# Kernel tuning notes

Measured on AMD Instinct MI355X. Metric: run time of the kernel, lower is better.

The kernel has to match this reference:

```python
import jax, jax.numpy as jnp
import numpy as np

B, T, H, U, F, K, M = 64, 2048, 1024, 128, 32, 31, 512
PAD = 2 * (K - 1) // 2  # dilation=2, 'same' padding = 30


def setup_inputs() -> dict:
    key = jax.random.key(0)
    ks = jax.random.split(key, 10)
    s = lambda d: 1.0 / np.sqrt(d)
    return {
        "query": jax.random.normal(ks[0], (B, 1, H), dtype=jnp.float32),
        "state": jax.random.uniform(ks[1], (B, T), dtype=jnp.float32),
        "prev_cum": jnp.zeros((B, T), dtype=jnp.float32),
        "memory": jax.random.normal(ks[2], (B, T, M), dtype=jnp.float32),
        "Wq": jax.random.normal(ks[3], (H, U), dtype=jnp.float32) * s(H),
        "bq": jnp.zeros((U,), dtype=jnp.float32),
        "Wm": jax.random.normal(ks[4], (M, U), dtype=jnp.float32) * s(M),
        "bm": jnp.zeros((U,), dtype=jnp.float32),
        "Wl": jax.random.normal(ks[5], (F, U), dtype=jnp.float32) * s(F),
        "bl": jnp.zeros((U,), dtype=jnp.float32),
        "We": jax.random.normal(ks[6], (U, U), dtype=jnp.float32) * s(U),
        "be": jnp.zeros((U,), dtype=jnp.float32),
        "va": jax.random.normal(ks[7], (U,), dtype=jnp.float32),
        "conv_w": jax.random.normal(ks[8], (F, 1, K), dtype=jnp.float32) * s(K),
        "conv_b": jnp.zeros((F,), dtype=jnp.float32),
    }


def reference(query, state, prev_cum, memory, Wq, bq, Wm, bm, Wl, bl, We, be, va, conv_w, conv_b):
    # query projection, keep first time step: [B,1,U]
    pq = (query @ Wq + bq)[:, 0:1, :]
    # processed memory (done in initialize() in torch): [B,T,U]
    pm = memory @ Wm + bm
    # location features: dilated conv over previous alignment, 'same' length
    x = state[:, None, :]  # [B,1,T]
    f = jax.lax.conv_general_dilated(
        x, conv_w, window_strides=(1,), padding=[(PAD, PAD)],
        rhs_dilation=(2,), dimension_numbers=("NCH", "OIH", "NCH"),
    ) + conv_b[None, :, None]                     # [B,F,T]
    pl = jnp.transpose(f, (0, 2, 1)) @ Wl + bl    # [B,T,U]
    # additive energy with extra linear + v_a reduction: [B,T]
    energy = jnp.sum(va * jnp.tanh((pq + pl + pm) @ We + be), axis=2)
    # smoothing (sigmoid) normalization instead of softmax
    sg = jax.nn.sigmoid(energy)
    alignment = sg / jnp.sum(sg, axis=-1, keepdims=True)  # [B,T]
    cum = prev_cum + alignment  # cumulate_weights=True
    # context over PROCESSED memory, matching self.memoery usage: [B,1,U]
    context = cum[:, None, :] @ pm
    return context
```

## Files before the change

kernel.cpp:

```cpp
#include <hip/hip_runtime.h>

#define Bv 64
#define Tv 2048
#define Hv 1024
#define Uv 128
#define Mv 512

typedef __bf16 bf16x8 __attribute__((ext_vector_type(8)));
typedef float f32x4 __attribute__((ext_vector_type(4)));

union U4BF { uint4 u; bf16x8 b; };

#define MFMA(a, b, c) __builtin_amdgcn_mfma_f32_16x16x32_bf16((a), (b), (c), 0, 0, 0)

#define GLOAD_LDS16(g, l) __builtin_amdgcn_global_load_lds( \
    (const __attribute__((address_space(1))) unsigned int*)(g), \
    (__attribute__((address_space(3))) unsigned int*)(l), 16, 0, 0)

__device__ __forceinline__ unsigned short f2bf(float f) {
  __bf16 h = (__bf16)f;
  return __builtin_bit_cast(unsigned short, h);
}
__device__ __forceinline__ unsigned int pack2(unsigned short lo, unsigned short hi) {
  return (unsigned int)lo | ((unsigned int)hi << 16);
}

__global__ __launch_bounds__(128) void k1_kernel(const float* __restrict__ query,
                                                 const float* __restrict__ Wq,
                                                 const float* __restrict__ bq,
                                                 const float* __restrict__ Wl,
                                                 const float* __restrict__ bl,
                                                 const float* __restrict__ conv_w,
                                                 const float* __restrict__ conv_b,
                                                 float* __restrict__ pq,
                                                 float* __restrict__ W2,
                                                 float* __restrict__ bias2) {
  const int bx = blockIdx.x;
  const int u = threadIdx.x;
  if (bx < 512) {
    const int b = bx >> 3, c = bx & 7;
    float acc = (c == 0) ? bq[u] : 0.0f;
    const float* q  = query + b * Hv + c * 128;
    const float* wq = Wq + (size_t)c * 128 * Uv;
    #pragma unroll 8
    for (int h = 0; h < 128; ++h) acc = fmaf(q[h], wq[h * Uv + u], acc);
    unsafeAtomicAdd(&pq[b * Uv + u], acc);
  } else {
    float wl[32];
    #pragma unroll
    for (int f = 0; f < 32; ++f) wl[f] = Wl[f * Uv + u];
    for (int k = 0; k < 31; ++k) {
      float acc = 0.0f;
      #pragma unroll
      for (int f = 0; f < 32; ++f) acc = fmaf(conv_w[f * 31 + k], wl[f], acc);
      W2[k * Uv + u] = acc;
    }
    float acc = bl[u];
    #pragma unroll
    for (int f = 0; f < 32; ++f) acc = fmaf(conv_b[f], wl[f], acc);
    bias2[u] = acc;
  }
}

__global__ __launch_bounds__(256) void k2_kernel(const float* __restrict__ pq,
                                                 const float* __restrict__ bias2,
                                                 const float* __restrict__ bm,
                                                 const float* __restrict__ be,
                                                 const float* __restrict__ We,
                                                 const float* __restrict__ W2,
                                                 float* __restrict__ qe,
                                                 float* __restrict__ w3tmp) {
  const int gtid = blockIdx.x * 256 + threadIdx.x;
  const int r = gtid >> 7, n = gtid & 127;
  if (r < 64) {
    float acc = be[n];
    for (int u = 0; u < Uv; ++u)
      acc = fmaf(pq[r * Uv + u] + bias2[u] + bm[u], We[u * Uv + n], acc);
    qe[r * Uv + n] = acc;
  } else {
    const int w = r - 64;
    float acc = 0.0f;
    if (w < 31) {
      for (int u = 0; u < Uv; ++u) acc = fmaf(W2[w * Uv + u], We[u * Uv + n], acc);
    }
    w3tmp[w * Uv + n] = acc;
  }
}

__global__ __launch_bounds__(256) void k3_kernel(const float* __restrict__ Wm,
                                                 const float* __restrict__ We,
                                                 const float* __restrict__ w3tmp,
                                                 unsigned short* __restrict__ WmF,
                                                 unsigned short* __restrict__ WeF,
                                                 unsigned short* __restrict__ W3F) {
  const int gtid = blockIdx.x * 256 + threadIdx.x;
  const int fid = gtid >> 6, lane = gtid & 63;
  const int quad = lane >> 4, l4 = lane & 15;
  float v[8];
  unsigned short* dst;
  if (fid < 128) {
    const int kc = fid >> 3, uj = fid & 7;
    #pragma unroll
    for (int j = 0; j < 8; ++j) v[j] = Wm[(size_t)(kc * 32 + quad * 8 + j) * Uv + uj * 16 + l4];
    dst = WmF + (size_t)fid * 512 + lane * 8;
  } else if (fid < 160) {
    const int f2 = fid - 128;
    const int kc = f2 >> 3, nj = f2 & 7;
    #pragma unroll
    for (int j = 0; j < 8; ++j) v[j] = We[(size_t)(kc * 32 + quad * 8 + j) * Uv + nj * 16 + l4];
    dst = WeF + (size_t)f2 * 512 + lane * 8;
  } else {
    const int nj = fid - 160;
    #pragma unroll
    for (int j = 0; j < 8; ++j) v[j] = w3tmp[(quad * 8 + j) * Uv + nj * 16 + l4];
    dst = W3F + (size_t)nj * 512 + lane * 8;
  }
  uint4 o;
  o.x = pack2(f2bf(v[0]), f2bf(v[1]));
  o.y = pack2(f2bf(v[2]), f2bf(v[3]));
  o.z = pack2(f2bf(v[4]), f2bf(v[5]));
  o.w = pack2(f2bf(v[6]), f2bf(v[7]));
  *(uint4*)dst = o;
}

__global__ __launch_bounds__(256) void main_kernel(
    const float* __restrict__ memory, const unsigned short* __restrict__ WmF,
    const unsigned short* __restrict__ WeF, const unsigned short* __restrict__ W3F,
    const float* __restrict__ qe, const float* __restrict__ state,
    const float* __restrict__ prev_cum, const float* __restrict__ bm,
    const float* __restrict__ va,
    float* __restrict__ P0, float* __restrict__ P1, float* __restrict__ Ssg) {
  const int tid = threadIdx.x;
  const int lane = tid & 63, wid = tid >> 6;
  const int l4 = lane & 15, quad = lane >> 4;
  const int wt = wid >> 1, wu = wid & 1;
  const int b = blockIdx.y, t0 = blockIdx.x * 64;

  __shared__ float sState[124];
  __shared__ float sPc[64];
  __shared__ float sBm[128];
  __shared__ float sVa[128];
  __shared__ float sSg[64];
  __shared__ float blkP0[128], blkP1[128];
  __shared__ float blkSsg;
  __shared__ __align__(16) unsigned short sS[64 * 144];
  __shared__ __align__(16) float sA[2][2048];

  const int p0 = tid, p1 = tid + 256;
  const int sr0 = p0 >> 3, sc0 = (p0 & 7) ^ (sr0 & 7);
  const int sr1 = p1 >> 3, sc1 = (p1 & 7) ^ (sr1 & 7);
  const float* g0 = memory + ((size_t)b * Tv + t0 + sr0) * Mv + sc0 * 4;
  const float* g1 = memory + ((size_t)b * Tv + t0 + sr1) * Mv + sc1 * 4;

  {
    float* d0 = &sA[0][0] + wid * 256;
    GLOAD_LDS16(g0, d0);
    GLOAD_LDS16(g1, d0 + 1024);
  }

  const unsigned short* bBase = WmF + (size_t)(wu * 4) * 512 + lane * 8;
  uint4 bc0 = *(const uint4*)(bBase);
  uint4 bc1 = *(const uint4*)(bBase + 512);
  uint4 bc2 = *(const uint4*)(bBase + 1024);
  uint4 bc3 = *(const uint4*)(bBase + 1536);

  for (int i = tid; i < 124; i += 256) {
    int t = t0 - 30 + i;
    sState[i] = (t >= 0 && t < Tv) ? state[b * Tv + t] : 0.0f;
  }
  if (tid < 64) sPc[tid] = prev_cum[b * Tv + t0 + tid];
  for (int i = tid; i < 128; i += 256) {
    sBm[i] = bm[i]; sVa[i] = va[i]; blkP0[i] = 0.0f; blkP1[i] = 0.0f;
  }
  if (tid == 0) blkSsg = 0.0f;

  const int r0 = wt * 32 + l4;
  const int q2 = quad * 2, rx = r0 & 7;
  const int s00 = r0 * 8 + (q2 ^ rx);
  const int s01 = r0 * 8 + ((q2 + 1) ^ rx);

  f32x4 acc[2][4];
  #pragma unroll
  for (int ti = 0; ti < 2; ++ti)
    #pragma unroll
    for (int uj = 0; uj < 4; ++uj) acc[ti][uj] = (f32x4){0.f, 0.f, 0.f, 0.f};

  __syncthreads();

  for (int kc = 0; kc < 16; ++kc) {
    const int cur = kc & 1;
    if (kc < 15) {
      float* d0 = &sA[0][0] + (cur ? 0 : 2048) + wid * 256;
      GLOAD_LDS16(g0 + (kc + 1) * 32, d0);
      GLOAD_LDS16(g1 + (kc + 1) * 32, d0 + 1024);
    }
    uint4 bn0, bn1, bn2, bn3;
    if (kc < 15) {
      const unsigned short* nb = bBase + (size_t)(kc + 1) * 8 * 512;
      bn0 = *(const uint4*)(nb);
      bn1 = *(const uint4*)(nb + 512);
      bn2 = *(const uint4*)(nb + 1024);
      bn3 = *(const uint4*)(nb + 1536);
    }
    const float4* sf = (const float4*)(&sA[0][0]) + (cur ? 512 : 0);
    float4 a0 = sf[s00];
    float4 a1 = sf[s01];
    float4 a2 = sf[s00 + 128];
    float4 a3 = sf[s01 + 128];
    bf16x8 af0, af1;
    af0[0] = (__bf16)a0.x; af0[1] = (__bf16)a0.y; af0[2] = (__bf16)a0.z; af0[3] = (__bf16)a0.w;
    af0[4] = (__bf16)a1.x; af0[5] = (__bf16)a1.y; af0[6] = (__bf16)a1.z; af0[7] = (__bf16)a1.w;
    af1[0] = (__bf16)a2.x; af1[1] = (__bf16)a2.y; af1[2] = (__bf16)a2.z; af1[3] = (__bf16)a2.w;
    af1[4] = (__bf16)a3.x; af1[5] = (__bf16)a3.y; af1[6] = (__bf16)a3.z; af1[7] = (__bf16)a3.w;
    U4BF bb0, bb1, bb2, bb3;
    bb0.u = bc0; bb1.u = bc1; bb2.u = bc2; bb3.u = bc3;
    acc[0][0] = MFMA(af0, bb0.b, acc[0][0]);
    acc[1][0] = MFMA(af1, bb0.b, acc[1][0]);
    acc[0][1] = MFMA(af0, bb1.b, acc[0][1]);
    acc[1][1] = MFMA(af1, bb1.b, acc[1][1]);
    acc[0][2] = MFMA(af0, bb2.b, acc[0][2]);
    acc[1][2] = MFMA(af1, bb2.b, acc[1][2]);
    acc[0][3] = MFMA(af0, bb3.b, acc[0][3]);
    acc[1][3] = MFMA(af1, bb3.b, acc[1][3]);
    if (kc < 15) {
      bc0 = bn0; bc1 = bn1; bc2 = bn2; bc3 = bn3;
      __syncthreads();
    }
  }

  #pragma unroll
  for (int ti = 0; ti < 2; ++ti) {
    const int rowb = wt * 32 + ti * 16 + quad * 4;
    #pragma unroll
    for (int uj = 0; uj < 4; ++uj) {
      const int col = wu * 64 + uj * 16 + l4;
      #pragma unroll
      for (int r = 0; r < 4; ++r) sS[(rowb + r) * 144 + col] = f2bf(acc[ti][uj][r]);
    }
  }
  __syncthreads();

  const int w = wid;
  f32x4 e[8];
  #pragma unroll
  for (int nj = 0; nj < 8; ++nj) {
    float qv = qe[b * Uv + nj * 16 + l4];
    e[nj] = (f32x4){qv, qv, qv, qv};
  }
  bf16x8 a2f;
  #pragma unroll
  for (int j = 0; j < 8; ++j) {
    int k = quad * 8 + j;
    float v = (k < 31) ? sState[(w * 16 + l4) + 2 * k] : 0.0f;
    a2f[j] = (__bf16)v;
  }
  #pragma unroll
  for (int nj = 0; nj < 8; ++nj) {
    U4BF bb; bb.u = *(const uint4*)(W3F + (size_t)nj * 512 + lane * 8);
    e[nj] = MFMA(a2f, bb.b, e[nj]);
  }
  #pragma unroll
  for (int ks = 0; ks < 4; ++ks) {
    U4BF au;
    au.u = *(const uint4*)&sS[(w * 16 + l4) * 144 + ks * 32 + quad * 8];
    #pragma unroll
    for (int nj = 0; nj < 8; ++nj) {
      U4BF bb; bb.u = *(const uint4*)(WeF + (size_t)(ks * 8 + nj) * 512 + lane * 8);
      e[nj] = MFMA(au.b, bb.b, e[nj]);
    }
  }
  float p[4] = {0.f, 0.f, 0.f, 0.f};
  #pragma unroll
  for (int nj = 0; nj < 8; ++nj) {
    float vav = sVa[nj * 16 + l4];
    #pragma unroll
    for (int r = 0; r < 4; ++r) p[r] = fmaf(vav, tanhf(e[nj][r]), p[r]);
  }
  #pragma unroll
  for (int off = 1; off <= 8; off <<= 1) {
    #pragma unroll
    for (int r = 0; r < 4; ++r) p[r] += __shfl_xor(p[r], off, 64);
  }
  float sgv4[4], sgsum = 0.f;
  #pragma unroll
  for (int r = 0; r < 4; ++r) {
    sgv4[r] = 1.0f / (1.0f + expf(-p[r]));
    sgsum += sgv4[r];
  }
  if (l4 == 0) {
    #pragma unroll
    for (int r = 0; r < 4; ++r) sSg[w * 16 + quad * 4 + r] = sgv4[r];
    atomicAdd(&blkSsg, sgsum);
  }
  __syncthreads();

  float sgl[8], pcl[8];
  #pragma unroll
  for (int ti = 0; ti < 2; ++ti)
    #pragma unroll
    for (int r = 0; r < 4; ++r) {
      int row = wt * 32 + ti * 16 + quad * 4 + r;
      sgl[ti * 4 + r] = sSg[row];
      pcl[ti * 4 + r] = sPc[row];
    }
  #pragma unroll
  for (int uj = 0; uj < 4; ++uj) {
    const int col = wu * 64 + uj * 16 + l4;
    const float bmv = sBm[col];
    float c0 = 0.f, c1 = 0.f;
    #pragma unroll
    for (int ti = 0; ti < 2; ++ti)
      #pragma unroll
      for (int r = 0; r < 4; ++r) {
        float pmv = acc[ti][uj][r] + bmv;
        c0 = fmaf(pcl[ti * 4 + r], pmv, c0);
        c1 = fmaf(sgl[ti * 4 + r], pmv, c1);
      }
    c0 += __shfl_xor(c0, 16, 64); c0 += __shfl_xor(c0, 32, 64);
    c1 += __shfl_xor(c1, 16, 64); c1 += __shfl_xor(c1, 32, 64);
    if (quad == 0) {
      atomicAdd(&blkP0[col], c0);
      atomicAdd(&blkP1[col], c1);
    }
  }
  __syncthreads();
  if (tid < 128) {
    unsafeAtomicAdd(&P0[b * Uv + tid], blkP0[tid]);
    unsafeAtomicAdd(&P1[b * Uv + tid], blkP1[tid]);
  }
  if (tid == 0) unsafeAtomicAdd(&Ssg[b], blkSsg);
}

__global__ __launch_bounds__(128) void finish_kernel(const float* __restrict__ P0,
                                                     const float* __restrict__ P1,
                                                     const float* __restrict__ Ssg,
                                                     float* __restrict__ out) {
  const int b = blockIdx.x, u = threadIdx.x;
  out[b * Uv + u] = P0[b * Uv + u] + P1[b * Uv + u] / Ssg[b];
}

extern "C" void kernel_launch(void* const* d_in, const int* in_sizes, int n_in,
                              void* d_out, int out_size, void* d_ws, size_t ws_size,
                              hipStream_t stream) {
  (void)in_sizes; (void)n_in; (void)out_size; (void)ws_size;
  const float* query    = (const float*)d_in[0];
  const float* state    = (const float*)d_in[1];
  const float* prev_cum = (const float*)d_in[2];
  const float* memory   = (const float*)d_in[3];
  const float* Wq       = (const float*)d_in[4];
  const float* bq       = (const float*)d_in[5];
  const float* Wm       = (const float*)d_in[6];
  const float* bm       = (const float*)d_in[7];
  const float* Wl       = (const float*)d_in[8];
  const float* bl       = (const float*)d_in[9];
  const float* We       = (const float*)d_in[10];
  const float* be       = (const float*)d_in[11];
  const float* va       = (const float*)d_in[12];
  const float* conv_w   = (const float*)d_in[13];
  const float* conv_b   = (const float*)d_in[14];

  float* ws = (float*)d_ws;
  float* P0    = ws;
  float* P1    = ws + 8192;
  float* Ssg   = ws + 16384;
  float* pq    = ws + 16448;
  float* W2    = ws + 24640;
  float* bias2 = ws + 28608;
  float* qe    = ws + 28736;
  float* w3tmp = ws + 36928;
  unsigned short* WmF = (unsigned short*)(ws + 41024);
  unsigned short* WeF = (unsigned short*)(ws + 73792);
  unsigned short* W3F = (unsigned short*)(ws + 81984);

  hipMemsetAsync(d_ws, 0, 24640 * sizeof(float), stream);

  k1_kernel<<<513, 128, 0, stream>>>(query, Wq, bq, Wl, bl, conv_w, conv_b, pq, W2, bias2);
  k2_kernel<<<48, 256, 0, stream>>>(pq, bias2, bm, be, We, W2, qe, w3tmp);
  k3_kernel<<<42, 256, 0, stream>>>(Wm, We, w3tmp, WmF, WeF, W3F);
  main_kernel<<<dim3(Tv / 64, Bv), 256, 0, stream>>>(
      memory, WmF, WeF, W3F, qe, state, prev_cum, bm, va, P0, P1, Ssg);
  finish_kernel<<<Bv, 128, 0, stream>>>(P0, P1, Ssg, (float*)d_out);
}
```

Baseline: 454.8 us.

## Split fused main kernel into projection and energy kernels via bf16 pm buffer

Splits the fused main kernel in two. The first kernel computes the memory projection pm and writes it to global memory as bf16. The second reloads that tile to compute energy, sigmoid and the context partials, using fast exp-based tanh and sigmoid. The aim is to lower register and LDS pressure per kernel so more blocks fit per CU, at the cost of an extra 32 MB bf16 round trip through global memory and an additional launch. The context now uses bf16-rounded pm instead of fp32 accumulators, which costs some accuracy.

After: 453.4 us. Within noise of the previous version (-0.3%).

```diff
diff --git a/kernel.cpp b/kernel.cpp
--- a/kernel.cpp
+++ b/kernel.cpp
@@ -21,8 +21,19 @@
   __bf16 h = (__bf16)f;
   return __builtin_bit_cast(unsigned short, h);
 }
+__device__ __forceinline__ float bf2f(unsigned short u) {
+  unsigned int x = ((unsigned int)u) << 16;
+  return __builtin_bit_cast(float, x);
+}
 __device__ __forceinline__ unsigned int pack2(unsigned short lo, unsigned short hi) {
   return (unsigned int)lo | ((unsigned int)hi << 16);
+}
+__device__ __forceinline__ float tanh_fast(float x) {
+  float e = __expf(2.0f * x);
+  return 1.0f - 2.0f / (e + 1.0f);
+}
+__device__ __forceinline__ float sigmoid_fast(float x) {
+  return 1.0f / (1.0f + __expf(-x));
 }
 
 __global__ __launch_bounds__(128) void k1_kernel(const float* __restrict__ query,
@@ -123,28 +134,18 @@
   *(uint4*)dst = o;
 }
 
-__global__ __launch_bounds__(256) void main_kernel(
+__global__ __launch_bounds__(256) void ph1_kernel(
     const float* __restrict__ memory, const unsigned short* __restrict__ WmF,
-    const unsigned short* __restrict__ WeF, const unsigned short* __restrict__ W3F,
-    const float* __restrict__ qe, const float* __restrict__ state,
-    const float* __restrict__ prev_cum, const float* __restrict__ bm,
-    const float* __restrict__ va,
-    float* __restrict__ P0, float* __restrict__ P1, float* __restrict__ Ssg) {
+    unsigned short* __restrict__ pm) {
   const int tid = threadIdx.x;
   const int lane = tid & 63, wid = tid >> 6;
   const int l4 = lane & 15, quad = lane >> 4;
   const int wt = wid >> 1, wu = wid & 1;
   const int b = blockIdx.y, t0 = blockIdx.x * 64;
 
-  __shared__ float sState[124];
-  __shared__ float sPc[64];
-  __shared__ float sBm[128];
-  __shared__ float sVa[128];
-  __shared__ float sSg[64];
-  __shared__ float blkP0[128], blkP1[128];
-  __shared__ float blkSsg;
-  __shared__ __align__(16) unsigned short sS[64 * 144];
-  __shared__ __align__(16) float sA[2][2048];
+  __shared__ __align__(16) char smem[18432];
+  float* sAf = (float*)smem;
+  unsigned short* sS = (unsigned short*)smem;
 
   const int p0 = tid, p1 = tid + 256;
   const int sr0 = p0 >> 3, sc0 = (p0 & 7) ^ (sr0 & 7);
@@ -153,10 +154,20 @@
   const float* g1 = memory + ((size_t)b * Tv + t0 + sr1) * Mv + sc1 * 4;
 
   {
-    float* d0 = &sA[0][0] + wid * 256;
-    GLOAD_LDS16(g0, d0);
-    GLOAD_LDS16(g1, d0 + 1024);
-  }
+    float* d = sAf + wid * 256;
+    GLOAD_LDS16(g0, d); GLOAD_LDS16(g1, d + 1024);
+  }
+
+  const int r0 = wt * 32 + l4;
+  const int q2 = quad * 2, rx = r0 & 7;
+  const int s00 = r0 * 8 + (q2 ^ rx);
+  const int s01 = r0 * 8 + ((q2 + 1) ^ rx);
+
+  f32x4 acc[2][4];
+  #pragma unroll
+  for (int ti = 0; ti < 2; ++ti)
+    #pragma unroll
+    for (int uj = 0; uj < 4; ++uj) acc[ti][uj] = (f32x4){0.f, 0.f, 0.f, 0.f};
 
   const unsigned short* bBase = WmF + (size_t)(wu * 4) * 512 + lane * 8;
   uint4 bc0 = *(const uint4*)(bBase);
@@ -164,45 +175,23 @@
   uint4 bc2 = *(const uint4*)(bBase + 1024);
   uint4 bc3 = *(const uint4*)(bBase + 1536);
 
-  for (int i = tid; i < 124; i += 256) {
-    int t = t0 - 30 + i;
-    sState[i] = (t >= 0 && t < Tv) ? state[b * Tv + t] : 0.0f;
-  }
-  if (tid < 64) sPc[tid] = prev_cum[b * Tv + t0 + tid];
-  for (int i = tid; i < 128; i += 256) {
-    sBm[i] = bm[i]; sVa[i] = va[i]; blkP0[i] = 0.0f; blkP1[i] = 0.0f;
-  }
-  if (tid == 0) blkSsg = 0.0f;
-
-  const int r0 = wt * 32 + l4;
-  const int q2 = quad * 2, rx = r0 & 7;
-  const int s00 = r0 * 8 + (q2 ^ rx);
-  const int s01 = r0 * 8 + ((q2 + 1) ^ rx);
-
-  f32x4 acc[2][4];
-  #pragma unroll
-  for (int ti = 0; ti < 2; ++ti)
-    #pragma unroll
-    for (int uj = 0; uj < 4; ++uj) acc[ti][uj] = (f32x4){0.f, 0.f, 0.f, 0.f};
-
   __syncthreads();
 
   for (int kc = 0; kc < 16; ++kc) {
     const int cur = kc & 1;
     if (kc < 15) {
-      float* d0 = &sA[0][0] + (cur ? 0 : 2048) + wid * 256;
-      GLOAD_LDS16(g0 + (kc + 1) * 32, d0);
-      GLOAD_LDS16(g1 + (kc + 1) * 32, d0 + 1024);
+      float* d = sAf + (cur ? 0 : 2048) + wid * 256;
+      GLOAD_LDS16(g0 + (kc + 1) * 32, d); GLOAD_LDS16(g1 + (kc + 1) * 32, d + 1024);
     }
     uint4 bn0, bn1, bn2, bn3;
     if (kc < 15) {
-      const unsigned short* nb = bBase + (size_t)(kc + 1) * 8 * 512;
+      const unsigned short* nb = bBase + (size_t)(kc + 1) * 4096;
       bn0 = *(const uint4*)(nb);
       bn1 = *(const uint4*)(nb + 512);
       bn2 = *(const uint4*)(nb + 1024);
       bn3 = *(const uint4*)(nb + 1536);
     }
-    const float4* sf = (const float4*)(&sA[0][0]) + (cur ? 512 : 0);
+    const float4* sf = (const float4*)(sAf) + (cur ? 512 : 0);
     float4 a0 = sf[s00];
     float4 a1 = sf[s01];
     float4 a2 = sf[s00 + 128];
@@ -212,21 +201,23 @@
     af0[4] = (__bf16)a1.x; af0[5] = (__bf16)a1.y; af0[6] = (__bf16)a1.z; af0[7] = (__bf16)a1.w;
     af1[0] = (__bf16)a2.x; af1[1] = (__bf16)a2.y; af1[2] = (__bf16)a2.z; af1[3] = (__bf16)a2.w;
     af1[4] = (__bf16)a3.x; af1[5] = (__bf16)a3.y; af1[6] = (__bf16)a3.z; af1[7] = (__bf16)a3.w;
-    U4BF bb0, bb1, bb2, bb3;
-    bb0.u = bc0; bb1.u = bc1; bb2.u = bc2; bb3.u = bc3;
-    acc[0][0] = MFMA(af0, bb0.b, acc[0][0]);
-    acc[1][0] = MFMA(af1, bb0.b, acc[1][0]);
-    acc[0][1] = MFMA(af0, bb1.b, acc[0][1]);
-    acc[1][1] = MFMA(af1, bb1.b, acc[1][1]);
-    acc[0][2] = MFMA(af0, bb2.b, acc[0][2]);
-    acc[1][2] = MFMA(af1, bb2.b, acc[1][2]);
-    acc[0][3] = MFMA(af0, bb3.b, acc[0][3]);
-    acc[1][3] = MFMA(af1, bb3.b, acc[1][3]);
+    U4BF u0, u1, u2, u3;
+    u0.u = bc0; u1.u = bc1; u2.u = bc2; u3.u = bc3;
+    acc[0][0] = MFMA(af0, u0.b, acc[0][0]);
+    acc[1][0] = MFMA(af1, u0.b, acc[1][0]);
+    acc[0][1] = MFMA(af0, u1.b, acc[0][1]);
+    acc[1][1] = MFMA(af1, u1.b, acc[1][1]);
+    acc[0][2] = MFMA(af0, u2.b, acc[0][2]);
+    acc[1][2] = MFMA(af1, u2.b, acc[1][2]);
+    acc[0][3] = MFMA(af0, u3.b, acc[0][3]);
+    acc[1][3] = MFMA(af1, u3.b, acc[1][3]);
     if (kc < 15) {
       bc0 = bn0; bc1 = bn1; bc2 = bn2; bc3 = bn3;
       __syncthreads();
     }
   }
+
+  __syncthreads();
 
   #pragma unroll
   for (int ti = 0; ti < 2; ++ti) {
@@ -240,6 +231,55 @@
   }
   __syncthreads();
 
+  const size_t baseT = (size_t)b * Tv + t0;
+  #pragma unroll
+  for (int i = 0; i < 4; ++i) {
+    const int idx = i * 256 + tid;
+    const int row = idx >> 4, c = idx & 15;
+    *(uint4*)&pm[(baseT + row) * Uv + c * 8] = *(const uint4*)&sS[row * 144 + c * 8];
+  }
+}
+
+__global__ __launch_bounds__(256) void ph23_kernel(
+    const unsigned short* __restrict__ pm, const unsigned short* __restrict__ WeF,
+    const unsigned short* __restrict__ W3F, const float* __restrict__ qe,
+    const float* __restrict__ state, const float* __restrict__ prev_cum,
+    const float* __restrict__ bm, const float* __restrict__ va,
+    float* __restrict__ P0, float* __restrict__ P1, float* __restrict__ Ssg) {
+  const int tid = threadIdx.x;
+  const int lane = tid & 63, wid = tid >> 6;
+  const int l4 = lane & 15, quad = lane >> 4;
+  const int wt = wid >> 1, wu = wid & 1;
+  const int b = blockIdx.y, t0 = blockIdx.x * 64;
+
+  __shared__ float sState[124];
+  __shared__ float sPc[64];
+  __shared__ float sBm[128];
+  __shared__ float sVa[128];
+  __shared__ float sSg[64];
+  __shared__ float blkP0[128], blkP1[128];
+  __shared__ float blkSsg;
+  __shared__ __align__(16) unsigned short sS[64 * 144];
+
+  for (int i = tid; i < 124; i += 256) {
+    int t = t0 - 30 + i;
+    sState[i] = (t >= 0 && t < Tv) ? state[b * Tv + t] : 0.0f;
+  }
+  if (tid < 64) sPc[tid] = prev_cum[b * Tv + t0 + tid];
+  for (int i = tid; i < 128; i += 256) {
+    sBm[i] = bm[i]; sVa[i] = va[i]; blkP0[i] = 0.0f; blkP1[i] = 0.0f;
+  }
+  if (tid == 0) blkSsg = 0.0f;
+
+  const size_t baseT = (size_t)b * Tv + t0;
+  #pragma unroll
+  for (int i = 0; i < 4; ++i) {
+    const int idx = i * 256 + tid;
+    const int row = idx >> 4, c = idx & 15;
+    *(uint4*)&sS[row * 144 + c * 8] = *(const uint4*)&pm[(baseT + row) * Uv + c * 8];
+  }
+  __syncthreads();
+
   const int w = wid;
   f32x4 e[8];
   #pragma unroll
@@ -274,7 +314,7 @@
   for (int nj = 0; nj < 8; ++nj) {
     float vav = sVa[nj * 16 + l4];
     #pragma unroll
-    for (int r = 0; r < 4; ++r) p[r] = fmaf(vav, tanhf(e[nj][r]), p[r]);
+    for (int r = 0; r < 4; ++r) p[r] = fmaf(vav, tanh_fast(e[nj][r]), p[r]);
   }
   #pragma unroll
   for (int off = 1; off <= 8; off <<= 1) {
@@ -284,7 +324,7 @@
   float sgv4[4], sgsum = 0.f;
   #pragma unroll
   for (int r = 0; r < 4; ++r) {
-    sgv4[r] = 1.0f / (1.0f + expf(-p[r]));
+    sgv4[r] = sigmoid_fast(p[r]);
     sgsum += sgv4[r];
   }
   if (l4 == 0) {
@@ -312,7 +352,8 @@
     for (int ti = 0; ti < 2; ++ti)
       #pragma unroll
       for (int r = 0; r < 4; ++r) {
-        float pmv = acc[ti][uj][r] + bmv;
+        const int row = wt * 32 + ti * 16 + quad * 4 + r;
+        float pmv = bf2f(sS[row * 144 + col]) + bmv;
         c0 = fmaf(pcl[ti * 4 + r], pmv, c0);
         c1 = fmaf(sgl[ti * 4 + r], pmv, c1);
       }
@@ -371,13 +412,15 @@
   unsigned short* WmF = (unsigned short*)(ws + 41024);
   unsigned short* WeF = (unsigned short*)(ws + 73792);
   unsigned short* W3F = (unsigned short*)(ws + 81984);
+  unsigned short* pm  = (unsigned short*)(ws + 84032);
 
   hipMemsetAsync(d_ws, 0, 24640 * sizeof(float), stream);
 
   k1_kernel<<<513, 128, 0, stream>>>(query, Wq, bq, Wl, bl, conv_w, conv_b, pq, W2, bias2);
   k2_kernel<<<48, 256, 0, stream>>>(pq, bias2, bm, be, We, W2, qe, w3tmp);
   k3_kernel<<<42, 256, 0, stream>>>(Wm, We, w3tmp, WmF, WeF, W3F);
-  main_kernel<<<dim3(Tv / 64, Bv), 256, 0, stream>>>(
-      memory, WmF, WeF, W3F, qe, state, prev_cum, bm, va, P0, P1, Ssg);
+  ph1_kernel<<<dim3(Tv / 64, Bv), 256, 0, stream>>>(memory, WmF, pm);
+  ph23_kernel<<<dim3(Tv / 64, Bv), 256, 0, stream>>>(
+      pm, WeF, W3F, qe, state, prev_cum, bm, va, P0, P1, Ssg);
   finish_kernel<<<Bv, 128, 0, stream>>>(P0, P1, Ssg, (float*)d_out);
 }
```
